# Kernel tuning notes

Hardware: AMD Instinct MI355X
Metric: run time of the kernel (lower is better)

## Reference

```python
import jax, jax.numpy as jnp
import numpy as np

DIM = 1024
NUM_HEADS = 16
HEAD_DIM = DIM // NUM_HEADS
SCALE = HEAD_DIM ** -0.5


def setup_inputs() -> dict:
    key = jax.random.key(0)
    k_x, k_qkv, k_proj, k_pb = jax.random.split(key, 4)
    B, N = 4, 2048
    x = jax.random.normal(k_x, (B, N, DIM), dtype=jnp.float32)
    # qkv: Linear(dim, 3*dim), qkv_bias=False -> no bias
    W_qkv = jax.random.normal(k_qkv, (DIM, 3 * DIM), dtype=jnp.float32) * (DIM ** -0.5)
    # proj: Linear(dim, dim) with bias (nn.Linear default)
    W_proj = jax.random.normal(k_proj, (DIM, DIM), dtype=jnp.float32) * (DIM ** -0.5)
    b_proj = jax.random.normal(k_pb, (DIM,), dtype=jnp.float32) * 0.01
    return {"x": x, "W_qkv": W_qkv, "W_proj": W_proj, "b_proj": b_proj}


def reference(x, W_qkv, W_proj, b_proj):
    B, N, C = x.shape
    H, D = NUM_HEADS, HEAD_DIM
    # qkv projection -> [B, N, 3, H, D] -> q,k,v each [B, H, N, D]
    qkv = (x @ W_qkv).reshape(B, N, 3, H, D)
    q, k, v = (jnp.moveaxis(qkv, 2, 0).transpose(0, 1, 3, 2, 4))  # [3,B,H,N,D]
    # attention scores [B, H, N, N], scaled QK^T (full matrix, as in source)
    attn = jnp.einsum('bhqd,bhkd->bhqk', q, k) * SCALE
    attn = jax.nn.softmax(attn, axis=-1)
    # attn @ V -> [B, H, N, D] -> [B, N, C]
    out = jnp.einsum('bhqk,bhkd->bhqd', attn, v)
    out = out.transpose(0, 2, 1, 3).reshape(B, N, C)
    # output projection
    return out @ W_proj + b_proj
```

## Files before the change

kernel.cpp:

```cpp
#include <hip/hip_runtime.h>
#include <hip/hip_bf16.h>

typedef __attribute__((ext_vector_type(8))) short short8;
typedef __attribute__((ext_vector_type(4))) short short4_t;
typedef __attribute__((ext_vector_type(4))) float floatx4;
typedef unsigned short u16;
typedef unsigned int u32;

#define SEQ 2048
#define NH 16
#define HD 64
#define CDIM 1024
#define MTOT 8192

__device__ __forceinline__ u16 f2bf(float f) {
  u32 u = __builtin_bit_cast(u32, f);
  u32 r = u + 0x7FFFu + ((u >> 16) & 1u);
  return (u16)(r >> 16);
}

__device__ __forceinline__ void gload16(const void* g, void* l) {
  __builtin_amdgcn_global_load_lds(
      (const __attribute__((address_space(1))) u32*)g,
      (__attribute__((address_space(3))) u32*)l, 16, 0, 0);
}

__global__ void cvt_x_kernel(const float* __restrict__ x, u16* __restrict__ xb) {
  size_t i = (size_t)blockIdx.x * 256 + threadIdx.x;
  const float4* xv = (const float4*)x;
  float4 a = xv[2 * i], c = xv[2 * i + 1];
  union { u16 h[8]; short8 v; } u;
  u.h[0] = f2bf(a.x); u.h[1] = f2bf(a.y); u.h[2] = f2bf(a.z); u.h[3] = f2bf(a.w);
  u.h[4] = f2bf(c.x); u.h[5] = f2bf(c.y); u.h[6] = f2bf(c.z); u.h[7] = f2bf(c.w);
  *(short8*)(xb + 8 * i) = u.v;
}

__global__ void transpose_w(const float* __restrict__ w, u16* __restrict__ wt,
                            int K, int N) {
  __shared__ float t[32][33];
  int n0 = blockIdx.x * 32, k0 = blockIdx.y * 32;
  int tr = threadIdx.x >> 5, tc = threadIdx.x & 31;
#pragma unroll
  for (int i = 0; i < 4; i++) {
    int r = tr + i * 8;
    t[r][tc] = w[(size_t)(k0 + r) * N + n0 + tc];
  }
  __syncthreads();
#pragma unroll
  for (int i = 0; i < 4; i++) {
    int r = tr + i * 8;
    wt[(size_t)(n0 + r) * K + k0 + tc] = f2bf(t[tc][r]);
  }
}

__global__ __launch_bounds__(256, 2) void gemm_qkv(
    const u16* __restrict__ A, const u16* __restrict__ BT,
    u16* __restrict__ qb, u16* __restrict__ kb, u16* __restrict__ vtb) {
  __shared__ u16 Ab[128 * 64];
  __shared__ u16 Bb[128 * 64];
  const int tid = threadIdx.x;
  const int w = tid >> 6, l = tid & 63;
  const int quad = l >> 4, l15 = l & 15;
  const int m0 = blockIdx.x * 128, n0 = blockIdx.y * 128;
  const int wr = w >> 1, wc = w & 1;

  floatx4 acc[4][4] = {};

  for (int k0 = 0; k0 < 1024; k0 += 64) {
    __syncthreads();
#pragma unroll
    for (int rnd = 0; rnd < 4; rnd++) {
      int ci = rnd * 256 + tid;
      int r = ci >> 3, pos = ci & 7;
      int c = pos ^ (r & 7);
      gload16(A + (size_t)(m0 + r) * 1024 + k0 + c * 8, (char*)Ab + ci * 16);
      gload16(BT + (size_t)(n0 + r) * 1024 + k0 + c * 8, (char*)Bb + ci * 16);
    }
    __syncthreads();
    short8 af[4][2], bf[4][2];
#pragma unroll
    for (int t = 0; t < 4; t++) {
      int ra = wr * 64 + t * 16 + l15;
      int ga = ra & 7;
#pragma unroll
      for (int ks = 0; ks < 2; ks++)
        af[t][ks] = *(short8*)((char*)Ab + ra * 128 + ((ks * 4 + quad) ^ ga) * 16);
      int rb = wc * 64 + t * 16 + l15;
      int gb = rb & 7;
#pragma unroll
      for (int ks = 0; ks < 2; ks++)
        bf[t][ks] = *(short8*)((char*)Bb + rb * 128 + ((ks * 4 + quad) ^ gb) * 16);
    }
#pragma unroll
    for (int ks = 0; ks < 2; ks++)
#pragma unroll
      for (int i = 0; i < 4; i++)
#pragma unroll
        for (int j = 0; j < 4; j++)
          acc[i][j] = __builtin_amdgcn_mfma_f32_16x16x32_bf16(af[i][ks], bf[j][ks], acc[i][j], 0, 0, 0);
  }

#pragma unroll
  for (int i = 0; i < 4; i++)
#pragma unroll
    for (int j = 0; j < 4; j++)
#pragma unroll
      for (int r = 0; r < 4; r++) {
        int m = m0 + wr * 64 + i * 16 + quad * 4 + r;
        int c = n0 + wc * 64 + j * 16 + l15;
        int b = m >> 11, n = m & 2047;
        int t = c >> 10, rem = c & 1023;
        int h = rem >> 6, d = rem & 63;
        int bh = b * NH + h;
        if (t == 0)      qb[((size_t)bh * SEQ + n) * HD + d] = f2bf(acc[i][j][r] * 0.18033688011112042f);
        else if (t == 1) kb[((size_t)bh * SEQ + n) * HD + d] = f2bf(acc[i][j][r]);
        else             vtb[((size_t)bh * HD + d) * SEQ + n] = f2bf(acc[i][j][r]);
      }
}

__global__ __launch_bounds__(256, 2) void gemm_proj(
    const u16* __restrict__ A, const u16* __restrict__ BT,
    const float* __restrict__ bias, float* __restrict__ out) {
  __shared__ u16 Ab[128 * 64];
  __shared__ u16 Bb[128 * 64];
  const int tid = threadIdx.x;
  const int w = tid >> 6, l = tid & 63;
  const int quad = l >> 4, l15 = l & 15;
  const int m0 = blockIdx.x * 128, n0 = blockIdx.y * 128;
  const int wr = w >> 1, wc = w & 1;

  floatx4 acc[4][4] = {};

  for (int k0 = 0; k0 < 1024; k0 += 64) {
    __syncthreads();
#pragma unroll
    for (int rnd = 0; rnd < 4; rnd++) {
      int ci = rnd * 256 + tid;
      int r = ci >> 3, pos = ci & 7;
      int c = pos ^ (r & 7);
      gload16(A + (size_t)(m0 + r) * 1024 + k0 + c * 8, (char*)Ab + ci * 16);
      gload16(BT + (size_t)(n0 + r) * 1024 + k0 + c * 8, (char*)Bb + ci * 16);
    }
    __syncthreads();
    short8 af[4][2], bf[4][2];
#pragma unroll
    for (int t = 0; t < 4; t++) {
      int ra = wr * 64 + t * 16 + l15;
      int ga = ra & 7;
#pragma unroll
      for (int ks = 0; ks < 2; ks++)
        af[t][ks] = *(short8*)((char*)Ab + ra * 128 + ((ks * 4 + quad) ^ ga) * 16);
      int rb = wc * 64 + t * 16 + l15;
      int gb = rb & 7;
#pragma unroll
      for (int ks = 0; ks < 2; ks++)
        bf[t][ks] = *(short8*)((char*)Bb + rb * 128 + ((ks * 4 + quad) ^ gb) * 16);
    }
#pragma unroll
    for (int ks = 0; ks < 2; ks++)
#pragma unroll
      for (int i = 0; i < 4; i++)
#pragma unroll
        for (int j = 0; j < 4; j++)
          acc[i][j] = __builtin_amdgcn_mfma_f32_16x16x32_bf16(af[i][ks], bf[j][ks], acc[i][j], 0, 0, 0);
  }

#pragma unroll
  for (int i = 0; i < 4; i++)
#pragma unroll
    for (int j = 0; j < 4; j++)
#pragma unroll
      for (int r = 0; r < 4; r++) {
        int m = m0 + wr * 64 + i * 16 + quad * 4 + r;
        int c = n0 + wc * 64 + j * 16 + l15;
        out[(size_t)m * CDIM + c] = acc[i][j][r] + bias[c];
      }
}

__global__ __launch_bounds__(512, 4) void attn_kernel(
    const u16* __restrict__ Qb, const u16* __restrict__ Kb,
    const u16* __restrict__ Vtb, u16* __restrict__ attnb) {
  __shared__ char smem[65536];
  const int tid = threadIdx.x;
  const int w = tid >> 6, l = tid & 63;
  const int quad = l >> 4, l15 = l & 15;

  const int lb = blockIdx.x + (blockIdx.y << 3);
  const int bh = ((lb & 7) << 3) + ((lb >> 3) & 7);
  const int qt0 = (lb >> 6) * 256;

  const u16* Kbase = Kb + (size_t)bh * SEQ * HD;
  const u16* Vbase = Vtb + (size_t)bh * HD * SEQ;

  short8 qf[2][2];
#pragma unroll
  for (int rt = 0; rt < 2; rt++) {
    int qrow = qt0 + w * 32 + rt * 16 + l15;
#pragma unroll
    for (int ks = 0; ks < 2; ks++)
      qf[rt][ks] = *(const short8*)(Qb + ((size_t)bh * SEQ + qrow) * HD + ks * 32 + quad * 8);
  }

  floatx4 O[2][4] = {};
  floatx4 sumacc[2] = {};

  union { u16 h[8]; short8 v; } onesu;
#pragma unroll
  for (int z = 0; z < 8; z++) onesu.h[z] = 0x3F80;
  const short8 ones = onesu.v;

  auto stage = [&](int n0, char* base) {
#pragma unroll
    for (int rnd = 0; rnd < 2; rnd++) {
      int ci = rnd * 512 + tid;
      int r = ci >> 3, pos = ci & 7;
      int c = pos ^ ((r & 7) ^ ((r >> 1) & 4));
      gload16(Kbase + (size_t)(n0 + r) * HD + c * 8, base + ci * 16);
    }
#pragma unroll
    for (int rnd = 0; rnd < 2; rnd++) {
      int ci = rnd * 512 + tid;
      int r = ci >> 4, pos = ci & 15;
      int c = pos ^ (r & 15);
      gload16(Vbase + (size_t)r * SEQ + n0 + c * 8, base + 16384 + ci * 16);
    }
  };

  stage(0, smem);
  __syncthreads();

  for (int kt = 0; kt < 16; kt++) {
    char* cur = smem + (kt & 1) * 32768;
    if (kt < 15) stage((kt + 1) * 128, smem + ((kt + 1) & 1) * 32768);

    char* KtC = cur;
    char* VtsC = cur + 16384;
#pragma unroll
    for (int p = 0; p < 4; p++) {
      floatx4 s[2][2];
#pragma unroll
      for (int t = 0; t < 2; t++) {
        int rho = p * 32 + (l15 >> 2) * 8 + t * 4 + (l15 & 3);
        int g = (rho & 7) ^ ((rho >> 1) & 4);
        short8 kf0 = *(short8*)(KtC + rho * 128 + ((0 + quad) ^ g) * 16);
        short8 kf1 = *(short8*)(KtC + rho * 128 + ((4 + quad) ^ g) * 16);
#pragma unroll
        for (int rt = 0; rt < 2; rt++) {
          floatx4 z = {};
          z = __builtin_amdgcn_mfma_f32_16x16x32_bf16(kf0, qf[rt][0], z, 0, 0, 0);
          z = __builtin_amdgcn_mfma_f32_16x16x32_bf16(kf1, qf[rt][1], z, 0, 0, 0);
          s[t][rt] = z;
        }
      }
      short8 pf[2];
#pragma unroll
      for (int rt = 0; rt < 2; rt++) {
        union { u32 d[4]; short8 v; } pu;
#pragma unroll
        for (int t = 0; t < 2; t++) {
          float e0 = __builtin_amdgcn_exp2f(s[t][rt][0]);
          float e1 = __builtin_amdgcn_exp2f(s[t][rt][1]);
          float e2 = __builtin_amdgcn_exp2f(s[t][rt][2]);
          float e3 = __builtin_amdgcn_exp2f(s[t][rt][3]);
          pu.d[t * 2 + 0] = __builtin_amdgcn_perm(
              __builtin_bit_cast(u32, e1), __builtin_bit_cast(u32, e0), 0x07060302u);
          pu.d[t * 2 + 1] = __builtin_amdgcn_perm(
              __builtin_bit_cast(u32, e3), __builtin_bit_cast(u32, e2), 0x07060302u);
        }
        pf[rt] = pu.v;
        sumacc[rt] = __builtin_amdgcn_mfma_f32_16x16x32_bf16(ones, pf[rt], sumacc[rt], 0, 0, 0);
      }
#pragma unroll
      for (int dt = 0; dt < 4; dt++) {
        int rv = dt * 16 + l15;
        short8 vf = *(short8*)(VtsC + rv * 256 + ((p * 4 + quad) ^ (rv & 15)) * 16);
#pragma unroll
        for (int rt = 0; rt < 2; rt++)
          O[rt][dt] = __builtin_amdgcn_mfma_f32_16x16x32_bf16(vf, pf[rt], O[rt][dt], 0, 0, 0);
      }
    }
    __syncthreads();
  }

  float inv[2];
#pragma unroll
  for (int rt = 0; rt < 2; rt++) inv[rt] = 1.f / sumacc[rt][0];

#pragma unroll
  for (int rt = 0; rt < 2; rt++)
#pragma unroll
    for (int dt = 0; dt < 4; dt++) {
      union { u16 h[4]; short4_t v; } pk;
#pragma unroll
      for (int r = 0; r < 4; r++) pk.h[r] = f2bf(O[rt][dt][r] * inv[rt]);
      *(short4_t*)(smem + (w * 32 + rt * 16 + l15) * 144 + (dt * 16 + quad * 4) * 2) = pk.v;
    }
  __syncthreads();
  {
    const int b = bh >> 4, h = bh & 15;
    int row = tid >> 1;
    int half = tid & 1;
    u16* gp = attnb + ((size_t)(b * SEQ + qt0 + row)) * CDIM + h * 64 + half * 32;
    char* lp = smem + row * 144 + half * 64;
#pragma unroll
    for (int c = 0; c < 4; c++)
      *(short8*)(gp + c * 8) = *(short8*)(lp + c * 16);
  }
}

extern "C" void kernel_launch(void* const* d_in, const int* in_sizes, int n_in,
                              void* d_out, int out_size, void* d_ws, size_t ws_size,
                              hipStream_t stream) {
  const float* x = (const float*)d_in[0];
  const float* Wqkv = (const float*)d_in[1];
  const float* Wproj = (const float*)d_in[2];
  const float* bproj = (const float*)d_in[3];
  float* out = (float*)d_out;

  u16* xb = (u16*)d_ws;
  u16* wqkvT = xb + (size_t)8388608;
  u16* wprojT = wqkvT + (size_t)3145728;
  u16* qb = wprojT + (size_t)1048576;
  u16* kb = qb + (size_t)8388608;
  u16* vtb = kb + (size_t)8388608;
  u16* attnb = xb;

  cvt_x_kernel<<<4096, 256, 0, stream>>>(x, xb);
  transpose_w<<<dim3(96, 32), 256, 0, stream>>>(Wqkv, wqkvT, 1024, 3072);
  transpose_w<<<dim3(32, 32), 256, 0, stream>>>(Wproj, wprojT, 1024, 1024);
  gemm_qkv<<<dim3(64, 24), 256, 0, stream>>>(xb, wqkvT, qb, kb, vtb);
  attn_kernel<<<dim3(8, 64), 512, 0, stream>>>(qb, kb, vtb, attnb);
  gemm_proj<<<dim3(64, 8), 256, 0, stream>>>(attnb, wprojT, bproj, out);
}
```

Before: 248.7 us.

## Enlarge QKV GEMM tile to 256x256 with double-buffered LDS pipeline

The QKV projection GEMM now uses 512-thread blocks computing 256x256 tiles, with two LDS buffers so the next K-tile's global-to-LDS loads overlap MFMA work on the current one. The inner loop is split into four phases with explicit barriers, waitcnt control and raised wave priority around the MFMA bursts. The aim is to cut per-iteration load stalls and raise operand reuse per LDS load. In exchange it uses 128KB of LDS and allows one block per CU, and the grid shrinks to 384 blocks, which may leave the 256 CUs unevenly loaded.

```diff
diff --git a/kernel.cpp b/kernel.cpp
--- a/kernel.cpp
+++ b/kernel.cpp
@@ -53,60 +53,88 @@
   }
 }
 
-__global__ __launch_bounds__(256, 2) void gemm_qkv(
+__global__ __launch_bounds__(512, 1) void gemm_qkv(
     const u16* __restrict__ A, const u16* __restrict__ BT,
     u16* __restrict__ qb, u16* __restrict__ kb, u16* __restrict__ vtb) {
-  __shared__ u16 Ab[128 * 64];
-  __shared__ u16 Bb[128 * 64];
+  __shared__ char smem[131072];
   const int tid = threadIdx.x;
   const int w = tid >> 6, l = tid & 63;
   const int quad = l >> 4, l15 = l & 15;
-  const int m0 = blockIdx.x * 128, n0 = blockIdx.y * 128;
-  const int wr = w >> 1, wc = w & 1;
-
-  floatx4 acc[4][4] = {};
-
-  for (int k0 = 0; k0 < 1024; k0 += 64) {
-    __syncthreads();
+  const int m0 = blockIdx.x * 256, n0 = blockIdx.y * 256;
+  const int wr = w >> 2, wc = w & 3;
+
+  floatx4 acc[8][4] = {};
+
+  auto stage = [&](int kt, int d) {
+    char* Ad = smem + d * 32768;
+    char* Bd = smem + 65536 + d * 32768;
 #pragma unroll
     for (int rnd = 0; rnd < 4; rnd++) {
-      int ci = rnd * 256 + tid;
+      int ci = rnd * 512 + tid;
       int r = ci >> 3, pos = ci & 7;
       int c = pos ^ (r & 7);
-      gload16(A + (size_t)(m0 + r) * 1024 + k0 + c * 8, (char*)Ab + ci * 16);
-      gload16(BT + (size_t)(n0 + r) * 1024 + k0 + c * 8, (char*)Bb + ci * 16);
-    }
-    __syncthreads();
-    short8 af[4][2], bf[4][2];
-#pragma unroll
-    for (int t = 0; t < 4; t++) {
-      int ra = wr * 64 + t * 16 + l15;
-      int ga = ra & 7;
+      gload16(A + (size_t)(m0 + r) * 1024 + kt * 64 + c * 8, Ad + ci * 16);
+      gload16(BT + (size_t)(n0 + r) * 1024 + kt * 64 + c * 8, Bd + ci * 16);
+    }
+  };
+
+  stage(0, 0);
+
+  for (int kt = 0; kt < 16; ++kt) {
+    const int cur = kt & 1;
+    if (kt < 15) stage(kt + 1, cur ^ 1);
+    __builtin_amdgcn_sched_barrier(0);
+    if (kt < 15) asm volatile("s_waitcnt vmcnt(8)" ::: "memory");
+    else         asm volatile("s_waitcnt vmcnt(0)" ::: "memory");
+    __builtin_amdgcn_s_barrier();
+    __builtin_amdgcn_sched_barrier(0);
+    char* Ab_ = smem + cur * 32768;
+    char* Bb_ = smem + 65536 + cur * 32768;
+#pragma unroll
+    for (int ph = 0; ph < 4; ++ph) {
+      const int mh = ph >> 1, nh = ph & 1;
+      short8 af[4][2], bf[2][2];
+#pragma unroll
+      for (int i = 0; i < 4; i++) {
+        int ra = wr * 128 + mh * 64 + i * 16 + l15;
+        int ga = ra & 7;
+#pragma unroll
+        for (int ks = 0; ks < 2; ks++)
+          af[i][ks] = *(short8*)(Ab_ + ra * 128 + ((ks * 4 + quad) ^ ga) * 16);
+      }
+#pragma unroll
+      for (int j = 0; j < 2; j++) {
+        int rb = wc * 64 + (nh * 2 + j) * 16 + l15;
+        int gb = rb & 7;
+#pragma unroll
+        for (int ks = 0; ks < 2; ks++)
+          bf[j][ks] = *(short8*)(Bb_ + rb * 128 + ((ks * 4 + quad) ^ gb) * 16);
+      }
+      __builtin_amdgcn_s_barrier();
+      asm volatile("s_waitcnt lgkmcnt(0)" ::: "memory");
+      __builtin_amdgcn_sched_barrier(0);
+      __builtin_amdgcn_s_setprio(1);
 #pragma unroll
       for (int ks = 0; ks < 2; ks++)
-        af[t][ks] = *(short8*)((char*)Ab + ra * 128 + ((ks * 4 + quad) ^ ga) * 16);
-      int rb = wc * 64 + t * 16 + l15;
-      int gb = rb & 7;
-#pragma unroll
-      for (int ks = 0; ks < 2; ks++)
-        bf[t][ks] = *(short8*)((char*)Bb + rb * 128 + ((ks * 4 + quad) ^ gb) * 16);
-    }
-#pragma unroll
-    for (int ks = 0; ks < 2; ks++)
-#pragma unroll
-      for (int i = 0; i < 4; i++)
-#pragma unroll
-        for (int j = 0; j < 4; j++)
-          acc[i][j] = __builtin_amdgcn_mfma_f32_16x16x32_bf16(af[i][ks], bf[j][ks], acc[i][j], 0, 0, 0);
-  }
-
-#pragma unroll
-  for (int i = 0; i < 4; i++)
+#pragma unroll
+        for (int i = 0; i < 4; i++)
+#pragma unroll
+          for (int j = 0; j < 2; j++)
+            acc[mh * 4 + i][nh * 2 + j] = __builtin_amdgcn_mfma_f32_16x16x32_bf16(
+                af[i][ks], bf[j][ks], acc[mh * 4 + i][nh * 2 + j], 0, 0, 0);
+      __builtin_amdgcn_s_setprio(0);
+      __builtin_amdgcn_s_barrier();
+      __builtin_amdgcn_sched_barrier(0);
+    }
+  }
+
+#pragma unroll
+  for (int i = 0; i < 8; i++)
 #pragma unroll
     for (int j = 0; j < 4; j++)
 #pragma unroll
       for (int r = 0; r < 4; r++) {
-        int m = m0 + wr * 64 + i * 16 + quad * 4 + r;
+        int m = m0 + wr * 128 + i * 16 + quad * 4 + r;
         int c = n0 + wc * 64 + j * 16 + l15;
         int b = m >> 11, n = m & 2047;
         int t = c >> 10, rem = c & 1023;
@@ -328,7 +356,7 @@
   cvt_x_kernel<<<4096, 256, 0, stream>>>(x, xb);
   transpose_w<<<dim3(96, 32), 256, 0, stream>>>(Wqkv, wqkvT, 1024, 3072);
   transpose_w<<<dim3(32, 32), 256, 0, stream>>>(Wproj, wprojT, 1024, 1024);
-  gemm_qkv<<<dim3(64, 24), 256, 0, stream>>>(xb, wqkvT, qb, kb, vtb);
+  gemm_qkv<<<dim3(32, 12), 512, 0, stream>>>(xb, wqkvT, qb, kb, vtb);
   attn_kernel<<<dim3(8, 64), 512, 0, stream>>>(qb, kb, vtb, attnb);
   gemm_proj<<<dim3(64, 8), 256, 0, stream>>>(attnb, wprojT, bproj, out);
 }
```

New measurement: 284.7 us. +14.5%, slower.
